# Optimization experiments

Measured on AMD Instinct MI355X. Metric: run time of the kernel, lower is better.

## Reference

```python
import jax, jax.numpy as jnp
import numpy as np

B, N, DIM = 2, 2048, 1024
HEADS, DIM_HEAD = 16, 64
SOFTCAP = 50.0
ROPE_THETA = 10000.0


def setup_inputs() -> dict:
    key = jax.random.key(0)
    k1, k2, k3 = jax.random.split(key, 3)
    x = jax.random.normal(k1, (B, N, DIM), jnp.float32)
    # structured modality positions: (type, offset, length), non-overlapping, in-bounds
    mods = np.zeros((B, 4, 3), np.int64)
    base_offsets = [200, 700, 1200, 1700]
    for b in range(B):
        for m, o in enumerate(base_offsets):
            mods[b, m] = (0, o + b * 16, 256)
    modalities = jnp.asarray(mods)
    gamma = jnp.zeros((DIM,), jnp.float32)           # RMSNorm gamma (init zeros, used as gamma+1)
    w_qkv = jax.random.normal(k2, (DIM, 3 * HEADS * DIM_HEAD), jnp.float32) * 0.02
    w_out = jax.random.normal(k3, (HEADS * DIM_HEAD, DIM), jnp.float32) * 0.02
    return {"x": x, "modalities": modalities, "gamma": gamma, "w_qkv": w_qkv, "w_out": w_out}


def _rotate_half(x):
    # interleaved-pair rotation, matching rotary-embedding-torch default
    x1, x2 = x[..., 0::2], x[..., 1::2]
    return jnp.stack((-x2, x1), axis=-1).reshape(x.shape)


def reference(x, modalities, gamma, w_qkv, w_out):
    b, n, d = x.shape
    h, dh = HEADS, DIM_HEAD
    seq = jnp.arange(n)
    off = modalities[..., 1]      # [b, m]
    length = modalities[..., 2]   # [b, m]

    # --- modality-aware rotary positions (span interior shrunk by offset [1, -1]) ---
    in_span = (seq[None, None, :] >= (off + 1)[:, :, None]) & (seq[None, None, :] < (off + length)[:, :, None])
    is_any_modality = in_span.any(axis=1)                                   # [b, n]
    pos = (seq[None, :] - jnp.cumsum(is_any_modality.astype(jnp.int32), axis=-1)).astype(jnp.float32)

    # --- RMSNorm: l2norm(x) * sqrt(d) * (gamma + 1) ---
    norm = jnp.maximum(jnp.sqrt(jnp.sum(x * x, axis=-1, keepdims=True)), 1e-12)
    xn = x / norm * jnp.sqrt(jnp.float32(d)) * (gamma + 1.0)

    # --- qkv projection, split heads -> [b, h, n, dh] ---
    qkv = (xn @ w_qkv).reshape(b, n, 3, h, dh)
    q, k, v = jnp.moveaxis(qkv, 2, 0)        # each [b, n, h, dh]
    q = jnp.transpose(q, (0, 2, 1, 3))
    k = jnp.transpose(k, (0, 2, 1, 3))
    v = jnp.transpose(v, (0, 2, 1, 3))

    # --- rotary embedding with modality-aware positions ---
    inv_freq = ROPE_THETA ** (-jnp.arange(0, dh, 2, dtype=jnp.float32) / dh)  # [dh/2]
    ang = pos[:, None, :, None] * inv_freq                                    # [b, 1, n, dh/2]
    ang = jnp.repeat(ang, 2, axis=-1)                                         # [b, 1, n, dh]
    cos, sin = jnp.cos(ang), jnp.sin(ang)
    q = q * cos + _rotate_half(q) * sin
    k = k * cos + _rotate_half(k) * sin

    # --- transfusion attention mask: causal OR per-modality bidirectional span ---
    causal_mask = seq[:, None] >= seq[None, :]                                 # [n, n]
    q_ge = seq[None, None, :] >= off[:, :, None]                               # [b, m, n]
    kv_lt = seq[None, None, :] < (off + length)[:, :, None]                    # [b, m, n]
    mod_mask = (q_ge[:, :, :, None] & kv_lt[:, :, None, :]).any(axis=1)        # [b, n, n]
    mask = causal_mask[None] | mod_mask                                        # [b, n, n]

    # --- attention with softclamp(50) ---
    scale = dh ** -0.5
    sim = jnp.einsum('bhid,bhjd->bhij', q, k) * scale
    sim = jnp.tanh(sim / SOFTCAP) * SOFTCAP
    sim = jnp.where(mask[:, None], sim, jnp.finfo(sim.dtype).min)
    attn = jax.nn.softmax(sim, axis=-1)
    out = jnp.einsum('bhij,bhjd->bhid', attn, v)                               # [b, h, n, dh]
    out = jnp.transpose(out, (0, 2, 1, 3)).reshape(b, n, h * dh)
    return out @ w_out
```

## Files before the change

kernel.cpp:

```cpp
#include <hip/hip_runtime.h>
#include <hip/hip_bf16.h>
#include <stdint.h>

#define B_ 2
#define N_ 2048
#define H_ 16
#define DIM_ 1024
#define NH3 3072
#define ROWS (B_*N_)

typedef __attribute__((ext_vector_type(8))) short bf16x8;
typedef __attribute__((ext_vector_type(4))) float f32x4;
typedef unsigned short u16;

__device__ __forceinline__ u16 f2bf(float f){
  union { float f; uint32_t u; } v; v.f = f;
  return (u16)((v.u + 0x7fffu + ((v.u >> 16) & 1u)) >> 16);
}

#if __has_builtin(__builtin_amdgcn_exp2f)
#define EXP2F(x) __builtin_amdgcn_exp2f(x)
#else
#define EXP2F(x) __expf((x) * 0.6931471805599453f)
#endif
#if __has_builtin(__builtin_amdgcn_rcpf)
#define RCPF(x) __builtin_amdgcn_rcpf(x)
#else
#define RCPF(x) (1.0f / (x))
#endif

#define GLL16(g, l) __builtin_amdgcn_global_load_lds( \
    (const __attribute__((address_space(1))) void*)(g), \
    (__attribute__((address_space(3))) void*)(l), 16, 0, 0)

__global__ void k_pos(const int* __restrict__ mods, float* __restrict__ pos){
  const int b = blockIdx.x;
  const int lane = threadIdx.x;
  int off[4], len[4];
#pragma unroll
  for (int m = 0; m < 4; ++m){
    off[m] = mods[(b*4 + m)*3 + 1];
    len[m] = mods[(b*4 + m)*3 + 2];
  }
  int run = 0;
  for (int c = 0; c < N_/64; ++c){
    int n = c*64 + lane;
    int v = 0;
#pragma unroll
    for (int m = 0; m < 4; ++m)
      if (n >= off[m] + 1 && n < off[m] + len[m]) v = 1;
    int s = v;
#pragma unroll
    for (int d = 1; d < 64; d <<= 1){
      int t = __shfl_up(s, d);
      if (lane >= d) s += t;
    }
    pos[b*N_ + n] = (float)(n - (run + s));
    run += __shfl(s, 63);
  }
}

__global__ void k_ropetab(const float* __restrict__ pos, float* __restrict__ cosT, float* __restrict__ sinT){
  int t = blockIdx.x*256 + threadIdx.x;
  if (t >= B_*N_*32) return;
  int f = t & 31, bn = t >> 5;
  float inv = powf(10000.0f, -(float)(2*f) / 64.0f);
  float ang = pos[bn] * inv;
  float s, c;
  sincosf(ang, &s, &c);
  cosT[t] = c; sinT[t] = s;
}

__global__ void k_transpose(const float* __restrict__ src, u16* __restrict__ dst, int R, int C){
  __shared__ float tile[32][33];
  int tx = threadIdx.x & 31, ty = threadIdx.x >> 5;
  int bc = blockIdx.x * 32, br = blockIdx.y * 32;
#pragma unroll
  for (int i = 0; i < 32; i += 8)
    tile[ty + i][tx] = src[(size_t)(br + ty + i)*C + bc + tx];
  __syncthreads();
#pragma unroll
  for (int i = 0; i < 32; i += 8)
    dst[(size_t)(bc + ty + i)*R + br + tx] = f2bf(tile[tx][ty + i]);
}

__global__ __launch_bounds__(256) void k_rmsnorm(const float* __restrict__ x, const float* __restrict__ gamma, u16* __restrict__ xn){
  int row = blockIdx.x, t = threadIdx.x;
  const float4 xv = ((const float4*)(x + (size_t)row*DIM_))[t];
  float ss = xv.x*xv.x + xv.y*xv.y + xv.z*xv.z + xv.w*xv.w;
#pragma unroll
  for (int d = 1; d < 64; d <<= 1) ss += __shfl_xor(ss, d);
  __shared__ float red[4];
  if ((t & 63) == 0) red[t >> 6] = ss;
  __syncthreads();
  float tot = red[0] + red[1] + red[2] + red[3];
  float scl = 32.0f / fmaxf(sqrtf(tot), 1e-12f);
  const float4 gv = ((const float4*)gamma)[t];
  ushort4 o;
  o.x = f2bf(xv.x * scl * (gv.x + 1.0f));
  o.y = f2bf(xv.y * scl * (gv.y + 1.0f));
  o.z = f2bf(xv.z * scl * (gv.z + 1.0f));
  o.w = f2bf(xv.w * scl * (gv.w + 1.0f));
  ((ushort4*)(xn + (size_t)row*DIM_))[t] = o;
}

template<int MODE, int BM>
__global__ __launch_bounds__(256) void k_gemm(
    const u16* __restrict__ A, const u16* __restrict__ Bt,
    int K, int Nc,
    float* __restrict__ outf,
    const float* __restrict__ cosT, const float* __restrict__ sinT,
    u16* __restrict__ qo, u16* __restrict__ ko, u16* __restrict__ vt)
{
  constexpr int MR = BM/32;
  constexpr int RA = BM/8;
  constexpr int CNT = (RA + 16)/4;
  __shared__ u16 lA[BM*64];
  __shared__ u16 lB[128*64];
  const int tid = threadIdx.x;
  const int wid = tid >> 6, lane = tid & 63;
  const int nx = gridDim.x;
  const int orig = blockIdx.y * nx + blockIdx.x;
  const int qq = (nx * gridDim.y) >> 3;
  const int wgid = (orig & 7) * qq + (orig >> 3);
  const int m0 = (wgid % nx) * BM, n0 = (wgid / nx) * 128;
  const int wm = wid >> 1, wn = wid & 1;
  const int srow = lane >> 3, sch = lane & 7;
  const int r16 = lane & 15, g4 = lane >> 4;
  f32x4 acc[MR][4] = {};
  const int ksteps = K >> 6;
  for (int kt = 0; kt < ksteps; ++kt){
    const int kb = kt*64;
    const int gch = sch ^ srow;
#pragma unroll
    for (int i = 0; i < CNT; ++i){
      const int reg = wid*CNT + i;
      if (reg < RA){
        const int row = reg*8 + srow;
        GLL16(A + (size_t)(m0 + row)*K + kb + gch*8, &lA[reg*512]);
      } else {
        const int r2 = reg - RA;
        const int row = r2*8 + srow;
        GLL16(Bt + (size_t)(n0 + row)*K + kb + gch*8, &lB[r2*512]);
      }
    }
    __syncthreads();
#pragma unroll
    for (int t = 0; t < 2; ++t){
      bf16x8 af[MR], bfr[4];
#pragma unroll
      for (int m = 0; m < MR; ++m){
        int row = wm*(BM/2) + m*16 + r16;
        int ch = (t*4 + g4) ^ (r16 & 7);
        af[m] = *(const bf16x8*)&lA[row*64 + ch*8];
      }
#pragma unroll
      for (int n = 0; n < 4; ++n){
        int row = wn*64 + n*16 + r16;
        int ch = (t*4 + g4) ^ (r16 & 7);
        bfr[n] = *(const bf16x8*)&lB[row*64 + ch*8];
      }
#pragma unroll
      for (int m = 0; m < MR; ++m)
#pragma unroll
        for (int n = 0; n < 4; ++n)
          acc[m][n] = __builtin_amdgcn_mfma_f32_16x16x32_bf16(af[m], bfr[n], acc[m][n], 0, 0, 0);
    }
    __syncthreads();
  }
#pragma unroll
  for (int m = 0; m < MR; ++m){
#pragma unroll
    for (int n = 0; n < 4; ++n){
      if constexpr (MODE == 0){
        const int gcol = n0 + wn*64 + n*16 + r16;
        const int s3 = gcol >> 10, hh = (gcol >> 6) & 15, d = gcol & 63;
        const int grow0 = m0 + wm*(BM/2) + m*16 + g4*4;
        const int b = grow0 >> 11, nn0 = grow0 & (N_-1);
        const size_t hb = (size_t)(b*H_ + hh);
        if (s3 == 2){
          uint32_t w01, w23;
          asm("v_cvt_pk_bf16_f32 %0, %1, %2" : "=v"(w01) : "v"(acc[m][n][0]), "v"(acc[m][n][1]));
          asm("v_cvt_pk_bf16_f32 %0, %1, %2" : "=v"(w23) : "v"(acc[m][n][2]), "v"(acc[m][n][3]));
          *reinterpret_cast<uint2*>(&vt[(hb*64 + d)*N_ + nn0]) = make_uint2(w01, w23);
        } else {
#pragma unroll
          for (int r = 0; r < 4; ++r){
            const float v = acc[m][n][r];
            const float part = __shfl_xor(v, 1);
            const int nn = nn0 + r;
            const int pidx = (b*N_ + nn)*32 + (d >> 1);
            const float c = cosT[pidx], sn = sinT[pidx];
            const float rot = (d & 1) ? (v*c + part*sn) : (v*c - part*sn);
            const u16 val = f2bf(rot);
            if (s3 == 0) qo[(hb*N_ + nn)*64 + d] = val;
            else         ko[(hb*N_ + nn)*64 + d] = val;
          }
        }
      } else {
#pragma unroll
        for (int r = 0; r < 4; ++r){
          const int grow = m0 + wm*(BM/2) + m*16 + g4*4 + r;
          const int gcol = n0 + wn*64 + n*16 + r16;
          outf[(size_t)grow*Nc + gcol] = acc[m][n][r];
        }
      }
    }
  }
}

#define PST 68
__global__ __launch_bounds__(256) void k_attn(
    const u16* __restrict__ qb, const u16* __restrict__ kb, const u16* __restrict__ vt,
    const int* __restrict__ mods, u16* __restrict__ xo)
{
  __shared__ u16 lK[64*64];
  __shared__ u16 lV[64*64];
  __shared__ u16 lP[4*16*PST];
  const int tid = threadIdx.x, wid = tid >> 6, lane = tid & 63;
  const int id = blockIdx.x;
  const int xcd = id & 7, slot = id >> 3;
  const int bh = xcd + 8*(slot & 3);
  const int qslot = slot >> 2;
  const int aa = qslot & 7, grp = qslot >> 3;
  const int qt = (grp == 0) ? aa : (grp == 1) ? (15 - aa) : (grp == 2) ? (16 + aa) : (31 - aa);
  const int b = bh >> 4, h = bh & 15;
  const int r16 = lane & 15, g4 = lane >> 4;
  const int srow = lane >> 3, sch = lane & 7;
  int moff[4], mend[4];
#pragma unroll
  for (int m = 0; m < 4; ++m){
    moff[m] = mods[(b*4+m)*3+1];
    mend[m] = moff[m] + mods[(b*4+m)*3+2];
  }
  const u16* kbase = kb + (size_t)bh*N_*64;
  const u16* vbase = vt + (size_t)bh*64*N_;
  u16* lPw = &lP[wid*16*PST];

  const int q0 = qt*64 + wid*16;
  const int i  = q0 + r16;
  const int imax = qt*64 + 63;
  int jmax = 0;
#pragma unroll
  for (int m = 0; m < 4; ++m)
    if (i >= moff[m]) jmax = max(jmax, mend[m]);
  const u16* qrow = qb + ((size_t)bh*N_ + q0 + r16)*64;
  const bf16x8 aq0 = *(const bf16x8*)&qrow[g4*8];
  const bf16x8 aq1 = *(const bf16x8*)&qrow[32 + g4*8];
  f32x4 o[4] = {};
  f32x4 acc_s = {};
  bf16x8 ones;
#pragma unroll
  for (int j = 0; j < 8; ++j) ones[j] = (short)0x3F80;

  const float D1 = 0.18033688011112043f;
  const float D3 = -3.7570183356483704e-07f;
  const float D5 = 9.392544618418597e-13f;

  for (int kt = 0; kt < N_/64; ++kt){
    bool proc = (kt*64 <= imax);
    if (!proc){
#pragma unroll
      for (int m = 0; m < 4; ++m)
        if (imax >= moff[m] && kt*64 < mend[m]) proc = true;
    }
    if (!proc) continue;
    __syncthreads();
#pragma unroll
    for (int ld = 0; ld < 2; ++ld){
      int reg = wid*2 + ld;
      int row = reg*8 + srow;
      int gch = sch ^ srow;
      GLL16(kbase + (size_t)(kt*64 + row)*64 + gch*8, &lK[reg*512]);
      GLL16(vbase + (size_t)row*N_ + kt*64 + gch*8,   &lV[reg*512]);
    }
    __syncthreads();
    f32x4 s[4] = {};
    __builtin_amdgcn_s_setprio(1);
#pragma unroll
    for (int cb = 0; cb < 4; ++cb){
#pragma unroll
      for (int t = 0; t < 2; ++t){
        int row = cb*16 + r16;
        int ch = (t*4 + g4) ^ (row & 7);
        bf16x8 bk = *(const bf16x8*)&lK[row*64 + ch*8];
        s[cb] = __builtin_amdgcn_mfma_f32_16x16x32_bf16(bk, t ? aq1 : aq0, s[cb], 0, 0, 0);
      }
    }
    __builtin_amdgcn_s_setprio(0);
    const int thr = max(i, jmax - 1) - kt*64;
    const bool nomask = (kt*64 + 63 <= q0);
#pragma unroll
    for (int cb = 0; cb < 4; ++cb){
      float p[4];
#pragma unroll
      for (int r = 0; r < 4; ++r){
        const float sv = s[cb][r];
        const float w = sv*sv;
        p[r] = EXP2F(sv * fmaf(w, fmaf(w, D5, D3), D1));
      }
      if (!nomask){
#pragma unroll
        for (int r = 0; r < 4; ++r)
          p[r] = (cb*16 + g4*4 + r <= thr) ? p[r] : 0.0f;
      }
      uint32_t w01, w23;
      asm("v_cvt_pk_bf16_f32 %0, %1, %2" : "=v"(w01) : "v"(p[0]), "v"(p[1]));
      asm("v_cvt_pk_bf16_f32 %0, %1, %2" : "=v"(w23) : "v"(p[2]), "v"(p[3]));
      *reinterpret_cast<uint2*>(&lPw[r16*PST + cb*16 + g4*4]) = make_uint2(w01, w23);
    }
    asm volatile("s_waitcnt lgkmcnt(0)" ::: "memory");
    __builtin_amdgcn_sched_barrier(0);
    union { uint2 h[2]; bf16x8 v; } u0, u1;
    u0.h[0] = *(const uint2*)&lPw[r16*PST + g4*8];
    u0.h[1] = *(const uint2*)&lPw[r16*PST + g4*8 + 4];
    u1.h[0] = *(const uint2*)&lPw[r16*PST + 32 + g4*8];
    u1.h[1] = *(const uint2*)&lPw[r16*PST + 32 + g4*8 + 4];
    __builtin_amdgcn_s_setprio(1);
    acc_s = __builtin_amdgcn_mfma_f32_16x16x32_bf16(u0.v, ones, acc_s, 0, 0, 0);
    acc_s = __builtin_amdgcn_mfma_f32_16x16x32_bf16(u1.v, ones, acc_s, 0, 0, 0);
#pragma unroll
    for (int cb = 0; cb < 4; ++cb){
#pragma unroll
      for (int t = 0; t < 2; ++t){
        int d = cb*16 + r16;
        int ch = (t*4 + g4) ^ (d & 7);
        bf16x8 bv = *(const bf16x8*)&lV[d*64 + ch*8];
        o[cb] = __builtin_amdgcn_mfma_f32_16x16x32_bf16(t ? u1.v : u0.v, bv, o[cb], 0, 0, 0);
      }
    }
    __builtin_amdgcn_s_setprio(0);
  }
#pragma unroll
  for (int r = 0; r < 4; ++r){
    const float linv = RCPF(acc_s[r]);
    const int iq = q0 + g4*4 + r;
#pragma unroll
    for (int cb = 0; cb < 4; ++cb)
      xo[(size_t)(b*N_ + iq)*DIM_ + h*64 + cb*16 + r16] = f2bf(o[cb][r]*linv);
  }
}

extern "C" void kernel_launch(void* const* d_in, const int* in_sizes, int n_in,
                              void* d_out, int out_size, void* d_ws, size_t ws_size,
                              hipStream_t stream){
  const float* x     = (const float*)d_in[0];
  const int*   mods  = (const int*)d_in[1];
  const float* gamma = (const float*)d_in[2];
  const float* wqkv  = (const float*)d_in[3];
  const float* wout  = (const float*)d_in[4];
  float* outp = (float*)d_out;

  char* p = (char*)d_ws;
  auto alloc = [&](size_t bytes) -> char* {
    char* r = p; p += (bytes + 255) & ~(size_t)255; return r;
  };
  float* pos   = (float*)alloc((size_t)B_*N_*4);
  float* cosT  = (float*)alloc((size_t)B_*N_*32*4);
  float* sinT  = (float*)alloc((size_t)B_*N_*32*4);
  u16* wqkvT   = (u16*)alloc((size_t)NH3*DIM_*2);
  u16* woutT   = (u16*)alloc((size_t)DIM_*DIM_*2);
  u16* xn      = (u16*)alloc((size_t)ROWS*DIM_*2);
  u16* qbb     = (u16*)alloc((size_t)B_*H_*N_*64*2);
  u16* kbb     = (u16*)alloc((size_t)B_*H_*N_*64*2);
  u16* vtb     = (u16*)alloc((size_t)B_*H_*N_*64*2);
  u16* xo      = (u16*)alloc((size_t)ROWS*DIM_*2);

  k_pos<<<B_, 64, 0, stream>>>(mods, pos);
  k_ropetab<<<(B_*N_*32 + 255)/256, 256, 0, stream>>>(pos, cosT, sinT);
  k_transpose<<<dim3(NH3/32, DIM_/32), 256, 0, stream>>>(wqkv, wqkvT, DIM_, NH3);
  k_transpose<<<dim3(DIM_/32, DIM_/32), 256, 0, stream>>>(wout, woutT, DIM_, DIM_);
  k_rmsnorm<<<ROWS, 256, 0, stream>>>(x, gamma, xn);
  k_gemm<0,128><<<dim3(ROWS/128, NH3/128), 256, 0, stream>>>(xn, wqkvT, DIM_, NH3, nullptr, cosT, sinT, qbb, kbb, vtb);
  k_attn<<<1024, 256, 0, stream>>>(qbb, kbb, vtb, mods, xo);
  k_gemm<1,64><<<dim3(ROWS/64, DIM_/128), 256, 0, stream>>>(xo, woutT, DIM_, DIM_, outp, nullptr, nullptr, nullptr, nullptr, nullptr);
}
```

Baseline: 134.6 us.

## Prefetch next K/V tile into registers while computing current tile

Replaces the per-tile direct global-to-LDS loads in the attention loop with a register prefetch. The next processed K/V tile is loaded into registers before the current tile's QK and PV MFMAs, then written to LDS after a barrier. The aim is to hide global memory latency behind compute. In exchange it uses more VGPRs, which may lower occupancy, and it still keeps two barriers per tile.

```diff
diff --git a/kernel.cpp b/kernel.cpp
--- a/kernel.cpp
+++ b/kernel.cpp
@@ -257,24 +257,36 @@
   const float D3 = -3.7570183356483704e-07f;
   const float D5 = 9.392544618418597e-13f;
 
-  for (int kt = 0; kt < N_/64; ++kt){
-    bool proc = (kt*64 <= imax);
-    if (!proc){
-#pragma unroll
-      for (int m = 0; m < 4; ++m)
-        if (imax >= moff[m] && kt*64 < mend[m]) proc = true;
-    }
-    if (!proc) continue;
-    __syncthreads();
-#pragma unroll
-    for (int ld = 0; ld < 2; ++ld){
-      int reg = wid*2 + ld;
-      int row = reg*8 + srow;
-      int gch = sch ^ srow;
-      GLL16(kbase + (size_t)(kt*64 + row)*64 + gch*8, &lK[reg*512]);
-      GLL16(vbase + (size_t)row*N_ + kt*64 + gch*8,   &lV[reg*512]);
-    }
-    __syncthreads();
+  auto proc = [&](int kt)->bool{
+    if (kt*64 <= imax) return true;
+    bool p = false;
+#pragma unroll
+    for (int m = 0; m < 4; ++m)
+      if (imax >= moff[m] && kt*64 < mend[m]) p = true;
+    return p;
+  };
+  const int gch = sch ^ srow;
+  const int reg0 = wid*2, reg1 = wid*2 + 1;
+
+  GLL16(kbase + (size_t)(reg0*8 + srow)*64 + gch*8, &lK[reg0*512]);
+  GLL16(kbase + (size_t)(reg1*8 + srow)*64 + gch*8, &lK[reg1*512]);
+  GLL16(vbase + (size_t)(reg0*8 + srow)*N_ + gch*8, &lV[reg0*512]);
+  GLL16(vbase + (size_t)(reg1*8 + srow)*N_ + gch*8, &lV[reg1*512]);
+  __syncthreads();
+
+  int kt = 0;
+  int nkt = 1;
+  while (nkt < 32 && !proc(nkt)) ++nkt;
+
+  while (true) {
+    uint4 kr0, kr1, vr0, vr1;
+    if (nkt < 32){
+      const u16* kp = kbase + (size_t)(nkt*64)*64;
+      kr0 = *(const uint4*)(kp + (size_t)(reg0*8 + srow)*64 + gch*8);
+      kr1 = *(const uint4*)(kp + (size_t)(reg1*8 + srow)*64 + gch*8);
+      vr0 = *(const uint4*)(vbase + (size_t)(reg0*8 + srow)*N_ + nkt*64 + gch*8);
+      vr1 = *(const uint4*)(vbase + (size_t)(reg1*8 + srow)*N_ + nkt*64 + gch*8);
+    }
     f32x4 s[4] = {};
     __builtin_amdgcn_s_setprio(1);
 #pragma unroll
@@ -330,6 +342,16 @@
       }
     }
     __builtin_amdgcn_s_setprio(0);
+    if (nkt >= 32) break;
+    __syncthreads();
+    *(uint4*)&lK[reg0*512 + lane*8] = kr0;
+    *(uint4*)&lK[reg1*512 + lane*8] = kr1;
+    *(uint4*)&lV[reg0*512 + lane*8] = vr0;
+    *(uint4*)&lV[reg1*512 + lane*8] = vr1;
+    __syncthreads();
+    kt = nkt;
+    ++nkt;
+    while (nkt < 32 && !proc(nkt)) ++nkt;
   }
 #pragma unroll
   for (int r = 0; r < 4; ++r){
```

After: 134.5 us. No clear change (-0.1%).
